# Kernel tuning notes

Measured on AMD Instinct MI355X. Metric: run time of the kernel, lower is better.

## Reference

```python
import jax, jax.numpy as jnp
import numpy as np

H_Q, H_KV, D_HEAD = 32, 4, 128

def setup_inputs() -> dict:
    key = jax.random.key(0)
    ks = jax.random.split(key, 5)
    B, S, H = 1, 4096, 2048
    hidden_states = jax.random.normal(ks[0], (B, S, H), jnp.float32)
    Wq = jax.random.normal(ks[1], (H, H_Q * D_HEAD), jnp.float32) * 0.02
    Wk = jax.random.normal(ks[2], (H, H_KV * D_HEAD), jnp.float32) * 0.02
    Wv = jax.random.normal(ks[3], (H, H_KV * D_HEAD), jnp.float32) * 0.02
    Wo = jax.random.normal(ks[4], (H_Q * D_HEAD, H), jnp.float32) * 0.02
    position_ids = jnp.arange(S, dtype=jnp.int32)
    # causal boolean mask, used as-is by the layer when rank != 2
    attention_mask = jnp.tril(jnp.ones((S, S), dtype=bool))[None, None]
    return dict(hidden_states=hidden_states, Wq=Wq, Wk=Wk, Wv=Wv, Wo=Wo,
                position_ids=position_ids, attention_mask=attention_mask)

def _rope(x, positions):
    # x: [B, S, H, D]; rotate-half style RoPE, max_wavelength=10000, scaling=1
    d = x.shape[-1]
    inv_freq = 1.0 / (10000.0 ** (jnp.arange(0, d, 2, dtype=jnp.float32) / d))  # [d/2]
    freq = positions.astype(jnp.float32)[:, None] * inv_freq[None, :]           # [S, d/2]
    emb = jnp.concatenate([freq, freq], axis=-1)                                # [S, d]
    cos = jnp.cos(emb)[None, :, None, :]
    sin = jnp.sin(emb)[None, :, None, :]
    x1, x2 = jnp.split(x, 2, axis=-1)
    rot = jnp.concatenate([-x2, x1], axis=-1)
    return x * cos + rot * sin

def reference(hidden_states, Wq, Wk, Wv, Wo, position_ids, attention_mask):
    B, S, H = hidden_states.shape
    q = (hidden_states @ Wq).reshape(B, S, H_Q, D_HEAD)
    k = (hidden_states @ Wk).reshape(B, S, H_KV, D_HEAD)
    v = (hidden_states @ Wv).reshape(B, S, H_KV, D_HEAD)
    q = _rope(q, position_ids)
    k = _rope(k, position_ids)
    q = q.transpose(0, 2, 1, 3)                                   # [B,Hq,S,D]
    num_groups = H_Q // H_KV
    k = jnp.repeat(k.transpose(0, 2, 1, 3), num_groups, axis=1)   # [B,Hq,S,D]
    v = jnp.repeat(v.transpose(0, 2, 1, 3), num_groups, axis=1)
    scores = jnp.einsum('bhqd,bhkd->bhqk', q, k) / jnp.sqrt(jnp.float32(D_HEAD))
    scores = jnp.where(attention_mask, scores, jnp.float32(-1e9))
    weights = jax.nn.softmax(scores, axis=-1)
    out = jnp.einsum('bhqk,bhkd->bhqd', weights, v)
    out = out.transpose(0, 2, 1, 3).reshape(B, S, H_Q * D_HEAD)
    return out @ Wo
```

## Files before the change

kernel.cpp:

```cpp
#include <hip/hip_runtime.h>
#include <hip/hip_bf16.h>

typedef __attribute__((ext_vector_type(8))) short bf16x8;
typedef __attribute__((ext_vector_type(4))) float f32x4;
typedef __attribute__((ext_vector_type(16))) float f32x16;

#define WAIT_VMCNT(n) asm volatile("s_waitcnt vmcnt(" #n ")" ::: "memory")
#define WAIT_LGKM0()  asm volatile("s_waitcnt lgkmcnt(0)" ::: "memory")

__device__ __forceinline__ unsigned short f2b(float f) {
  __hip_bfloat16 h = __float2bfloat16(f);
  return __builtin_bit_cast(unsigned short, h);
}
__device__ __forceinline__ float b2f(unsigned short u) {
  return __bfloat162float(__builtin_bit_cast(__hip_bfloat16, u));
}
__device__ __forceinline__ unsigned int pk2(float a, float b) {
  return (unsigned int)f2b(a) | ((unsigned int)f2b(b) << 16);
}

__device__ __forceinline__ void gld_lds16(const void* g, void* l) {
  __builtin_amdgcn_global_load_lds(
      (const __attribute__((address_space(1))) unsigned int*)g,
      (__attribute__((address_space(3))) unsigned int*)l, 16, 0, 0);
}

__global__ void convert_kernel(const float* __restrict__ in, unsigned short* __restrict__ out, int n4) {
  int i = blockIdx.x * blockDim.x + threadIdx.x;
  if (i >= n4) return;
  float4 v = ((const float4*)in)[i];
  ushort4 o;
  o.x = f2b(v.x); o.y = f2b(v.y); o.z = f2b(v.z); o.w = f2b(v.w);
  ((ushort4*)out)[i] = o;
}

__global__ void transpose_convert_kernel(const float* __restrict__ in, unsigned short* __restrict__ out,
                                         int R, int C) {
  __shared__ float tile[32][33];
  int c0 = blockIdx.x * 32, r0 = blockIdx.y * 32;
  int tx = threadIdx.x, ty = threadIdx.y;
#pragma unroll
  for (int k = 0; k < 32; k += 8)
    tile[ty + k][tx] = in[(size_t)(r0 + ty + k) * C + (c0 + tx)];
  __syncthreads();
#pragma unroll
  for (int k = 0; k < 32; k += 8)
    out[(size_t)(c0 + ty + k) * R + (r0 + tx)] = f2b(tile[tx][ty + k]);
}

__global__ void rope_kernel(unsigned short* __restrict__ buf, const int* __restrict__ pos,
                            int log2h, int rowstride, float outscale, int total) {
  int idx = blockIdx.x * blockDim.x + threadIdx.x;
  if (idx >= total) return;
  int i = idx & 63;
  int h = (idx >> 6) & ((1 << log2h) - 1);
  int s = idx >> (6 + log2h);
  float inv = expf(-0.14391156831212787f * (float)i);
  float f = (float)pos[s] * inv;
  float sn, cs;
  sincosf(f, &sn, &cs);
  unsigned short* p = buf + (size_t)s * rowstride + (h << 7) + i;
  float x1 = b2f(p[0]);
  float x2 = b2f(p[64]);
  p[0]  = f2b((x1 * cs - x2 * sn) * outscale);
  p[64] = f2b((x2 * cs + x1 * sn) * outscale);
}

template <int OUT_MODE>
__global__ __launch_bounds__(256) void gemm_bt_kernel(const unsigned short* __restrict__ A,
                                                      const unsigned short* __restrict__ Bt,
                                                      void* __restrict__ Cv,
                                                      void* __restrict__ C1,
                                                      void* __restrict__ C2,
                                                      int M, int N, int K) {
  __shared__ unsigned short As[2][128 * 32];
  __shared__ unsigned short Bs[2][128 * 32];
  int tid = threadIdx.x;
  int lane = tid & 63;
  int wave = tid >> 6;

  int nwg = gridDim.x * gridDim.y;
  int lin = blockIdx.y * gridDim.x + blockIdx.x;
  int cpx = nwg >> 3;
  int swz = (lin & 7) * cpx + (lin >> 3);
  int m0 = (swz / gridDim.x) * 128, n0 = (swz % gridDim.x) * 128;

  int wr = wave >> 1, wc = wave & 1;
  f32x4 acc[4][4] = {};

  int row0 = tid >> 2, cc0 = tid & 3;
  const unsigned short* pa0 = A + (size_t)(m0 + row0) * K + cc0 * 8;
  const unsigned short* pa1 = A + (size_t)(m0 + row0 + 64) * K + cc0 * 8;
  const unsigned short* pb0 = Bt + (size_t)(n0 + row0) * K + cc0 * 8;
  const unsigned short* pb1 = Bt + (size_t)(n0 + row0 + 64) * K + cc0 * 8;

  auto stage = [&](int b, int k0) {
    gld_lds16(pa0 + k0, (unsigned short*)As[b] + tid * 8);
    gld_lds16(pa1 + k0, (unsigned short*)As[b] + (256 + tid) * 8);
    gld_lds16(pb0 + k0, (unsigned short*)Bs[b] + tid * 8);
    gld_lds16(pb1 + k0, (unsigned short*)Bs[b] + (256 + tid) * 8);
  };

  int nk = K >> 5;
  stage(0, 0);
  stage(1, 32);
  for (int ki = 0; ki < nk; ++ki) {
    int cur = ki & 1;
    if (ki + 1 < nk) WAIT_VMCNT(4); else WAIT_VMCNT(0);
    __builtin_amdgcn_s_barrier();
    bf16x8 af[4], bfr[4];
#pragma unroll
    for (int mi = 0; mi < 4; ++mi) {
      int r = wr * 64 + mi * 16 + (lane & 15);
      af[mi] = *(const bf16x8*)((const char*)As[cur] + r * 64 + (lane >> 4) * 16);
    }
#pragma unroll
    for (int ni = 0; ni < 4; ++ni) {
      int r = wc * 64 + ni * 16 + (lane & 15);
      bfr[ni] = *(const bf16x8*)((const char*)Bs[cur] + r * 64 + (lane >> 4) * 16);
    }
#pragma unroll
    for (int mi = 0; mi < 4; ++mi)
#pragma unroll
      for (int ni = 0; ni < 4; ++ni)
        acc[mi][ni] = __builtin_amdgcn_mfma_f32_16x16x32_bf16(af[mi], bfr[ni], acc[mi][ni], 0, 0, 0);
    WAIT_LGKM0();
    __builtin_amdgcn_s_barrier();
    if (ki + 2 < nk) stage(cur, (ki + 2) * 32);
  }

#pragma unroll
  for (int mi = 0; mi < 4; ++mi) {
#pragma unroll
    for (int ni = 0; ni < 4; ++ni) {
      int col = n0 + wc * 64 + ni * 16 + (lane & 15);
      int rbase = m0 + wr * 64 + mi * 16 + (lane >> 4) * 4;
      if (OUT_MODE == 1) {
#pragma unroll
        for (int j = 0; j < 4; ++j)
          ((float*)Cv)[(size_t)(rbase + j) * N + col] = acc[mi][ni][j];
      } else {
        if (n0 < 4096) {
#pragma unroll
          for (int j = 0; j < 4; ++j)
            ((unsigned short*)Cv)[(size_t)(rbase + j) * 4096 + col] = f2b(acc[mi][ni][j]);
        } else if (n0 < 4608) {
          int c2 = col - 4096;
#pragma unroll
          for (int j = 0; j < 4; ++j)
            ((unsigned short*)C1)[(size_t)(rbase + j) * 512 + c2] = f2b(acc[mi][ni][j]);
        } else {
          int cv = col - 4608;
          int hk = cv >> 7, d = cv & 127;
          uint2 u;
          u.x = pk2(acc[mi][ni][0], acc[mi][ni][1]);
          u.y = pk2(acc[mi][ni][2], acc[mi][ni][3]);
          size_t addr = (size_t)hk * 524288 + (size_t)(rbase >> 6) * 8192 + d * 64 + (rbase & 63);
          *(uint2*)((unsigned short*)C2 + addr) = u;
        }
      }
    }
  }
}

__global__ __launch_bounds__(512) void attn_kernel(const unsigned short* __restrict__ Q,
                                                   const unsigned short* __restrict__ Kp,
                                                   const unsigned short* __restrict__ Vt,
                                                   unsigned short* __restrict__ O) {
  __shared__ unsigned short k_lds[2][64 * 128];
  __shared__ unsigned short vt_lds[2][128 * 64];

  int lin = blockIdx.y * 8 + blockIdx.x;
  int h = (lin & 7) * 4 + (lin >> 6);
  int xpair = (lin >> 3) & 7;
  int hk = h >> 3;
  int tid = threadIdx.x, lane = tid & 63, wave = tid >> 6;
  int l31 = lane & 31, hi = lane >> 5;

  int krow0 = tid >> 4, kch = tid & 15;
  int krow1 = krow0 + 32;
  const unsigned short* kp0 = Kp + (hk << 7) + (size_t)krow0 * 512 + ((kch ^ (krow0 & 15)) << 3);
  const unsigned short* kp1 = Kp + (hk << 7) + (size_t)krow1 * 512 + ((kch ^ (krow1 & 15)) << 3);
  int vd0 = tid >> 3, vsc = tid & 7;
  int vd1 = vd0 + 64;
  const unsigned short* vp0 = Vt + (size_t)hk * 524288 + vd0 * 64 + ((vsc ^ (vd0 & 7)) << 3);
  const unsigned short* vp1 = Vt + (size_t)hk * 524288 + vd1 * 64 + ((vsc ^ (vd1 & 7)) << 3);

  auto stage_tile = [&](int b, int t) {
    gld_lds16(kp0 + t * 32768, (unsigned short*)k_lds[b] + tid * 8);
    gld_lds16(kp1 + t * 32768, (unsigned short*)k_lds[b] + (512 + tid) * 8);
    gld_lds16(vp0 + t * 8192, (unsigned short*)vt_lds[b] + tid * 8);
    gld_lds16(vp1 + t * 8192, (unsigned short*)vt_lds[b] + (512 + tid) * 8);
  };

  for (int pass = 0; pass < 2; ++pass) {
    int SB = pass ? (15 - xpair) : xpair;
    int qt = SB * 8 + wave;
    int qrow = qt * 32 + l31;
    int tdiag = qt >> 1;
    int ntiles = 4 * SB + 4;

    bf16x8 qf[8];
#pragma unroll
    for (int kk = 0; kk < 8; ++kk)
      qf[kk] = *(const bf16x8*)(Q + (size_t)qrow * 4096 + (h << 7) + kk * 16 + hi * 8);

    f32x16 o_acc[4] = {};
    float m_run = -3.0e38f, l_run = 0.0f;

    __syncthreads();
    stage_tile(0, 0);
    stage_tile(1, 1);
    for (int t0 = 0; t0 < ntiles; ++t0) {
      int cur = t0 & 1;
      if (t0 + 1 < ntiles) WAIT_VMCNT(4); else WAIT_VMCNT(0);
      __builtin_amdgcn_s_barrier();

      if (t0 <= tdiag) {
        int s0 = t0 * 64;
        f32x16 sacc[2] = {};
        __builtin_amdgcn_s_setprio(1);
#pragma unroll
        for (int kk = 0; kk < 8; ++kk) {
#pragma unroll
          for (int t = 0; t < 2; ++t) {
            bf16x8 kf = *(const bf16x8*)((const char*)k_lds[cur] +
                         ((t * 32 + l31) * 256 + (((kk * 2 + hi) ^ (l31 & 15)) << 4)));
            sacc[t] = __builtin_amdgcn_mfma_f32_32x32x16_bf16(kf, qf[kk], sacc[t], 0, 0, 0);
          }
        }
        __builtin_amdgcn_s_setprio(0);

        float mx = -3.0e38f;
        if (t0 == tdiag) {
#pragma unroll
          for (int t = 0; t < 2; ++t)
#pragma unroll
            for (int r = 0; r < 16; ++r) {
              int sg = s0 + t * 32 + (r & 3) + 8 * (r >> 2) + 4 * hi;
              float v = sacc[t][r];
              v = (sg <= qrow) ? v : -3.0e38f;
              sacc[t][r] = v;
              mx = fmaxf(mx, v);
            }
        } else {
#pragma unroll
          for (int t = 0; t < 2; ++t)
#pragma unroll
            for (int r = 0; r < 16; ++r)
              mx = fmaxf(mx, sacc[t][r]);
        }
        mx = fmaxf(mx, __shfl_xor(mx, 32));
        if (!__all(mx <= m_run + 11.5416f)) {
          float m_new = fmaxf(m_run, mx);
          float corr = exp2f(m_run - m_new);
          l_run *= corr;
#pragma unroll
          for (int ds = 0; ds < 4; ++ds)
#pragma unroll
            for (int r = 0; r < 16; ++r) o_acc[ds][r] *= corr;
          m_run = m_new;
        }
        float rsum = 0.0f;
#pragma unroll
        for (int t = 0; t < 2; ++t)
#pragma unroll
          for (int r = 0; r < 16; ++r) {
            float e = exp2f(sacc[t][r] - m_run);
            sacc[t][r] = e;
            rsum += e;
          }
        l_run += rsum + __shfl_xor(rsum, 32);

        bf16x8 pb[4];
#pragma unroll
        for (int kk = 0; kk < 4; ++kk) {
          int t = kk >> 1;
          int b0 = (kk & 1) * 8;
          unsigned int a0 = pk2(sacc[t][b0 + 0], sacc[t][b0 + 1]);
          unsigned int a1 = pk2(sacc[t][b0 + 2], sacc[t][b0 + 3]);
          unsigned int c0 = pk2(sacc[t][b0 + 4], sacc[t][b0 + 5]);
          unsigned int c1 = pk2(sacc[t][b0 + 6], sacc[t][b0 + 7]);
          unsigned int snd0 = hi ? a0 : c0, snd1 = hi ? a1 : c1;
          unsigned int rcv0 = __shfl_xor(snd0, 32);
          unsigned int rcv1 = __shfl_xor(snd1, 32);
          unsigned int own0 = hi ? c0 : a0, own1 = hi ? c1 : a1;
          uint4 w;
          w.x = hi ? rcv0 : own0;
          w.y = hi ? rcv1 : own1;
          w.z = hi ? own0 : rcv0;
          w.w = hi ? own1 : rcv1;
          pb[kk] = __builtin_bit_cast(bf16x8, w);
        }

        __builtin_amdgcn_s_setprio(1);
#pragma unroll
        for (int ds = 0; ds < 4; ++ds) {
#pragma unroll
          for (int kk = 0; kk < 4; ++kk) {
            bf16x8 vf = *(const bf16x8*)((const char*)vt_lds[cur] +
                         ((ds * 32 + l31) * 128 + (((kk * 2 + hi) ^ (l31 & 7)) << 4)));
            o_acc[ds] = __builtin_amdgcn_mfma_f32_32x32x16_bf16(vf, pb[kk], o_acc[ds], 0, 0, 0);
          }
        }
        __builtin_amdgcn_s_setprio(0);
      }
      WAIT_LGKM0();
      __builtin_amdgcn_s_barrier();
      if (t0 + 2 < ntiles) stage_tile(cur, t0 + 2);
    }

    float inv_l = 1.0f / l_run;
    char* scr = (char*)k_lds + wave * 2304;
#pragma unroll
    for (int ds = 0; ds < 4; ++ds) {
#pragma unroll
      for (int rp = 0; rp < 8; ++rp) {
        int r = rp * 2;
        int d_loc = (r & 3) + 8 * (r >> 2) + 4 * hi;
        *(unsigned int*)(scr + l31 * 72 + ((d_loc >> 1) << 2)) =
            pk2(o_acc[ds][r] * inv_l, o_acc[ds][r + 1] * inv_l);
      }
      uint2 u0 = *(uint2*)(scr + l31 * 72 + hi * 32 + 0);
      uint2 u1 = *(uint2*)(scr + l31 * 72 + hi * 32 + 8);
      uint2 u2 = *(uint2*)(scr + l31 * 72 + hi * 32 + 16);
      uint2 u3 = *(uint2*)(scr + l31 * 72 + hi * 32 + 24);
      unsigned short* op = O + (size_t)qrow * 4096 + (h << 7) + ds * 32 + hi * 16;
      uint4 s0v; s0v.x = u0.x; s0v.y = u0.y; s0v.z = u1.x; s0v.w = u1.y;
      uint4 s1v; s1v.x = u2.x; s1v.y = u2.y; s1v.z = u3.x; s1v.w = u3.y;
      *(uint4*)(op) = s0v;
      *(uint4*)(op + 8) = s1v;
    }
  }
}

extern "C" void kernel_launch(void* const* d_in, const int* in_sizes, int n_in,
                              void* d_out, int out_size, void* d_ws, size_t ws_size,
                              hipStream_t stream) {
  const float* X  = (const float*)d_in[0];
  const float* Wq = (const float*)d_in[1];
  const float* Wk = (const float*)d_in[2];
  const float* Wv = (const float*)d_in[3];
  const float* Wo = (const float*)d_in[4];
  const int* pos  = (const int*)d_in[5];

  const size_t MB = 1u << 20;
  char* w = (char*)d_ws;
  unsigned short* Xb  = (unsigned short*)(w + 0 * MB);
  unsigned short* Wqt = (unsigned short*)(w + 16 * MB);
  unsigned short* Wkt = (unsigned short*)(w + 32 * MB);
  unsigned short* Wvt = (unsigned short*)(w + 34 * MB);
  unsigned short* Wot = (unsigned short*)(w + 36 * MB);
  unsigned short* Qb  = (unsigned short*)(w + 52 * MB);
  unsigned short* Kb  = (unsigned short*)(w + 84 * MB);
  unsigned short* Vtb = (unsigned short*)(w + 88 * MB);
  unsigned short* Ob  = (unsigned short*)(w + 92 * MB);

  convert_kernel<<<8192, 256, 0, stream>>>(X, Xb, 4096 * 2048 / 4);
  transpose_convert_kernel<<<dim3(128, 64), dim3(32, 8), 0, stream>>>(Wq, Wqt, 2048, 4096);
  transpose_convert_kernel<<<dim3(16, 64),  dim3(32, 8), 0, stream>>>(Wk, Wkt, 2048, 512);
  transpose_convert_kernel<<<dim3(16, 64),  dim3(32, 8), 0, stream>>>(Wv, Wvt, 2048, 512);
  transpose_convert_kernel<<<dim3(64, 128), dim3(32, 8), 0, stream>>>(Wo, Wot, 4096, 2048);

  gemm_bt_kernel<3><<<dim3(40, 32), 256, 0, stream>>>(Xb, Wqt, Qb, Kb, Vtb, 4096, 5120, 2048);

  rope_kernel<<<(4096 * 32 * 64) / 256, 256, 0, stream>>>(Qb, pos, 5, 4096, 0.12752792534390558f, 4096 * 32 * 64);
  rope_kernel<<<(4096 * 4 * 64) / 256,  256, 0, stream>>>(Kb, pos, 2, 512, 1.0f, 4096 * 4 * 64);

  attn_kernel<<<dim3(8, 32), 512, 0, stream>>>(Qb, Kb, Vtb, Ob);

  gemm_bt_kernel<1><<<dim3(16, 32), 256, 0, stream>>>(Ob, Wot, d_out, nullptr, nullptr, 4096, 2048, 4096);
}
```

Baseline: 449.7 us.

## Split attention blocks to 4 waves with 512 blocks and remapped head/slot scheduling

The attention kernel moves from 256 blocks of 8 waves (256 query rows each) to 512 blocks of 4 waves (128 query rows each). The block-to-head mapping is rewritten so each XCD handles 4 heads, and causal work is still balanced by pairing slots. Staging is redone so 256 threads issue 4 K and 4 V loads each, with the vmcnt wait raised to match. Smaller blocks should fill the 256 CUs more evenly and raise occupancy, but each K/V tile now serves half as many query rows, which doubles the tile loads per query row.

```diff
diff --git a/kernel.cpp b/kernel.cpp
--- a/kernel.cpp
+++ b/kernel.cpp
@@ -163,42 +163,49 @@
   }
 }
 
-__global__ __launch_bounds__(512) void attn_kernel(const unsigned short* __restrict__ Q,
+__global__ __launch_bounds__(256) void attn_kernel(const unsigned short* __restrict__ Q,
                                                    const unsigned short* __restrict__ Kp,
                                                    const unsigned short* __restrict__ Vt,
                                                    unsigned short* __restrict__ O) {
   __shared__ unsigned short k_lds[2][64 * 128];
   __shared__ unsigned short vt_lds[2][128 * 64];
 
-  int lin = blockIdx.y * 8 + blockIdx.x;
-  int h = (lin & 7) * 4 + (lin >> 6);
-  int xpair = (lin >> 3) & 7;
+  int lin = blockIdx.x;
+  int xcd = lin & 7;
+  int rest = lin >> 3;
+  int h = xcd * 4 + (rest & 3);
+  int slot = rest >> 2;
+
   int hk = h >> 3;
   int tid = threadIdx.x, lane = tid & 63, wave = tid >> 6;
   int l31 = lane & 31, hi = lane >> 5;
 
-  int krow0 = tid >> 4, kch = tid & 15;
-  int krow1 = krow0 + 32;
-  const unsigned short* kp0 = Kp + (hk << 7) + (size_t)krow0 * 512 + ((kch ^ (krow0 & 15)) << 3);
-  const unsigned short* kp1 = Kp + (hk << 7) + (size_t)krow1 * 512 + ((kch ^ (krow1 & 15)) << 3);
-  int vd0 = tid >> 3, vsc = tid & 7;
-  int vd1 = vd0 + 64;
-  const unsigned short* vp0 = Vt + (size_t)hk * 524288 + vd0 * 64 + ((vsc ^ (vd0 & 7)) << 3);
-  const unsigned short* vp1 = Vt + (size_t)hk * 524288 + vd1 * 64 + ((vsc ^ (vd1 & 7)) << 3);
+  const unsigned short* kpp[4];
+  const unsigned short* vpp[4];
+#pragma unroll
+  for (int it = 0; it < 4; ++it) {
+    int c = it * 256 + tid;
+    int row = c >> 4, ch = c & 15;
+    kpp[it] = Kp + (hk << 7) + (size_t)row * 512 + ((ch ^ (row & 15)) << 3);
+    int d = c >> 3, sc = c & 7;
+    vpp[it] = Vt + (size_t)hk * 524288 + d * 64 + ((sc ^ (d & 7)) << 3);
+  }
 
   auto stage_tile = [&](int b, int t) {
-    gld_lds16(kp0 + t * 32768, (unsigned short*)k_lds[b] + tid * 8);
-    gld_lds16(kp1 + t * 32768, (unsigned short*)k_lds[b] + (512 + tid) * 8);
-    gld_lds16(vp0 + t * 8192, (unsigned short*)vt_lds[b] + tid * 8);
-    gld_lds16(vp1 + t * 8192, (unsigned short*)vt_lds[b] + (512 + tid) * 8);
+#pragma unroll
+    for (int it = 0; it < 4; ++it)
+      gld_lds16(kpp[it] + t * 32768, (unsigned short*)k_lds[b] + (it * 256 + tid) * 8);
+#pragma unroll
+    for (int it = 0; it < 4; ++it)
+      gld_lds16(vpp[it] + t * 8192, (unsigned short*)vt_lds[b] + (it * 256 + tid) * 8);
   };
 
   for (int pass = 0; pass < 2; ++pass) {
-    int SB = pass ? (15 - xpair) : xpair;
-    int qt = SB * 8 + wave;
+    int SB = pass ? (31 - slot) : slot;
+    int qt = SB * 4 + wave;
     int qrow = qt * 32 + l31;
     int tdiag = qt >> 1;
-    int ntiles = 4 * SB + 4;
+    int ntiles = 2 * SB + 2;
 
     bf16x8 qf[8];
 #pragma unroll
@@ -213,7 +220,7 @@
     stage_tile(1, 1);
     for (int t0 = 0; t0 < ntiles; ++t0) {
       int cur = t0 & 1;
-      if (t0 + 1 < ntiles) WAIT_VMCNT(4); else WAIT_VMCNT(0);
+      if (t0 + 1 < ntiles) WAIT_VMCNT(8); else WAIT_VMCNT(0);
       __builtin_amdgcn_s_barrier();
 
       if (t0 <= tdiag) {
@@ -367,7 +374,7 @@
   rope_kernel<<<(4096 * 32 * 64) / 256, 256, 0, stream>>>(Qb, pos, 5, 4096, 0.12752792534390558f, 4096 * 32 * 64);
   rope_kernel<<<(4096 * 4 * 64) / 256,  256, 0, stream>>>(Kb, pos, 2, 512, 1.0f, 4096 * 4 * 64);
 
-  attn_kernel<<<dim3(8, 32), 512, 0, stream>>>(Qb, Kb, Vtb, Ob);
+  attn_kernel<<<512, 256, 0, stream>>>(Qb, Kb, Vtb, Ob);
 
   gemm_bt_kernel<1><<<dim3(16, 32), 256, 0, stream>>>(Ob, Wot, d_out, nullptr, nullptr, 4096, 2048, 4096);
 }
```

Result: slower. 555.2 us (+23.5%).

## Triple-buffer LDS in GEMM and attention to drop second barrier per tile

Applied to the files above, without the earlier changes.

Moves the GEMM and attention mainloops from double to triple LDS buffering. Prefetch of tile t+2 is issued right after the top-of-loop barrier into the third buffer, so the trailing lgkmcnt wait and second barrier per iteration can be removed. It also swaps the bf16 packing helper to the hardware packed convert instruction. The cost is 50% more LDS per block, which may lower occupancy, especially for the attention kernel (96KB).

```diff
diff --git a/kernel.cpp b/kernel.cpp
--- a/kernel.cpp
+++ b/kernel.cpp
@@ -6,7 +6,6 @@
 typedef __attribute__((ext_vector_type(16))) float f32x16;
 
 #define WAIT_VMCNT(n) asm volatile("s_waitcnt vmcnt(" #n ")" ::: "memory")
-#define WAIT_LGKM0()  asm volatile("s_waitcnt lgkmcnt(0)" ::: "memory")
 
 __device__ __forceinline__ unsigned short f2b(float f) {
   __hip_bfloat16 h = __float2bfloat16(f);
@@ -16,7 +15,9 @@
   return __bfloat162float(__builtin_bit_cast(__hip_bfloat16, u));
 }
 __device__ __forceinline__ unsigned int pk2(float a, float b) {
-  return (unsigned int)f2b(a) | ((unsigned int)f2b(b) << 16);
+  unsigned int r;
+  asm("v_cvt_pk_bf16_f32 %0, %1, %2" : "=v"(r) : "v"(a), "v"(b));
+  return r;
 }
 
 __device__ __forceinline__ void gld_lds16(const void* g, void* l) {
@@ -29,9 +30,10 @@
   int i = blockIdx.x * blockDim.x + threadIdx.x;
   if (i >= n4) return;
   float4 v = ((const float4*)in)[i];
-  ushort4 o;
-  o.x = f2b(v.x); o.y = f2b(v.y); o.z = f2b(v.z); o.w = f2b(v.w);
-  ((ushort4*)out)[i] = o;
+  uint2 o;
+  o.x = pk2(v.x, v.y);
+  o.y = pk2(v.z, v.w);
+  *(uint2*)(out + (size_t)i * 4) = o;
 }
 
 __global__ void transpose_convert_kernel(const float* __restrict__ in, unsigned short* __restrict__ out,
@@ -73,8 +75,8 @@
                                                       void* __restrict__ C1,
                                                       void* __restrict__ C2,
                                                       int M, int N, int K) {
-  __shared__ unsigned short As[2][128 * 32];
-  __shared__ unsigned short Bs[2][128 * 32];
+  __shared__ unsigned short As[3][128 * 32];
+  __shared__ unsigned short Bs[3][128 * 32];
   int tid = threadIdx.x;
   int lane = tid & 63;
   int wave = tid >> 6;
@@ -104,10 +106,14 @@
   int nk = K >> 5;
   stage(0, 0);
   stage(1, 32);
+  int cur = 0;
   for (int ki = 0; ki < nk; ++ki) {
-    int cur = ki & 1;
     if (ki + 1 < nk) WAIT_VMCNT(4); else WAIT_VMCNT(0);
     __builtin_amdgcn_s_barrier();
+    if (ki + 2 < nk) {
+      int b2 = cur + 2; if (b2 >= 3) b2 -= 3;
+      stage(b2, (ki + 2) * 32);
+    }
     bf16x8 af[4], bfr[4];
 #pragma unroll
     for (int mi = 0; mi < 4; ++mi) {
@@ -124,9 +130,7 @@
 #pragma unroll
       for (int ni = 0; ni < 4; ++ni)
         acc[mi][ni] = __builtin_amdgcn_mfma_f32_16x16x32_bf16(af[mi], bfr[ni], acc[mi][ni], 0, 0, 0);
-    WAIT_LGKM0();
-    __builtin_amdgcn_s_barrier();
-    if (ki + 2 < nk) stage(cur, (ki + 2) * 32);
+    cur = (cur == 2) ? 0 : cur + 1;
   }
 
 #pragma unroll
@@ -167,8 +171,8 @@
                                                    const unsigned short* __restrict__ Kp,
                                                    const unsigned short* __restrict__ Vt,
                                                    unsigned short* __restrict__ O) {
-  __shared__ unsigned short k_lds[2][64 * 128];
-  __shared__ unsigned short vt_lds[2][128 * 64];
+  __shared__ unsigned short k_lds[3][64 * 128];
+  __shared__ unsigned short vt_lds[3][128 * 64];
 
   int lin = blockIdx.y * 8 + blockIdx.x;
   int h = (lin & 7) * 4 + (lin >> 6);
@@ -211,10 +215,14 @@
     __syncthreads();
     stage_tile(0, 0);
     stage_tile(1, 1);
+    int cur = 0;
     for (int t0 = 0; t0 < ntiles; ++t0) {
-      int cur = t0 & 1;
       if (t0 + 1 < ntiles) WAIT_VMCNT(4); else WAIT_VMCNT(0);
       __builtin_amdgcn_s_barrier();
+      if (t0 + 2 < ntiles) {
+        int b2 = cur + 2; if (b2 >= 3) b2 -= 3;
+        stage_tile(b2, t0 + 2);
+      }
 
       if (t0 <= tdiag) {
         int s0 = t0 * 64;
@@ -305,10 +313,10 @@
         }
         __builtin_amdgcn_s_setprio(0);
       }
-      WAIT_LGKM0();
-      __builtin_amdgcn_s_barrier();
-      if (t0 + 2 < ntiles) stage_tile(cur, t0 + 2);
-    }
+      cur = (cur == 2) ? 0 : cur + 1;
+    }
+
+    __syncthreads();
 
     float inv_l = 1.0f / l_run;
     char* scr = (char*)k_lds + wave * 2304;
```

Result: no change. 445.3 us (-1.0%).
